# Kernel tuning notes

Measured on AMD Instinct MI355X. Metric: run time of the kernel, lower is better.

Reference implementation:

```python
import jax, jax.numpy as jnp
import numpy as np

EPS = 1e-4  # BatchNorm eps from module


def setup_inputs() -> dict:
    key = jax.random.key(0)
    ks = jax.random.split(key, 7)
    N, C, H, W = 4, 256, 64, 64
    D = C  # reduction=1
    x = jax.random.normal(ks[0], (N, C, H, W), dtype=jnp.float32)
    # 1x1 conv weights, msra-style scaled init
    s = 1.0 / np.sqrt(C)
    Wq = jax.random.normal(ks[1], (D, C), dtype=jnp.float32) * s
    Wk = jax.random.normal(ks[2], (D, C), dtype=jnp.float32) * s
    Wv = jax.random.normal(ks[3], (D, C), dtype=jnp.float32) * s
    Wo = jax.random.normal(ks[4], (C, D), dtype=jnp.float32) * s
    gamma = jnp.ones((C,), dtype=jnp.float32)
    beta = jnp.zeros((C,), dtype=jnp.float32)
    return {"x": x, "Wq": Wq, "Wk": Wk, "Wv": Wv, "Wo": Wo, "gamma": gamma, "beta": beta}


def reference(x, Wq, Wk, Wv, Wo, gamma, beta):
    N, C, H, W = x.shape
    D = Wq.shape[0]
    scale = 1.0 / jnp.sqrt(jnp.float32(D))
    xf = x.reshape(N, C, H * W)                      # (N, C, L)
    # 1x1 convs == per-position linear projections
    q = jnp.einsum('dc,ncl->nld', Wq, xf)            # (N, L, D)
    k = jnp.einsum('dc,ncl->nld', Wk, xf)            # (N, L, D)
    v = jnp.einsum('dc,ncl->nld', Wv, xf)            # (N, L, D)
    scores = jnp.einsum('nld,nmd->nlm', q, k) * scale  # (N, L, L)
    attn = jax.nn.softmax(scores, axis=2)
    out = jnp.einsum('nlm,nmd->nld', attn, v)        # (N, L, D)
    out = jnp.einsum('od,nld->nol', Wo, out).reshape(N, C, H, W)
    # BatchNorm2d (training-mode batch statistics, biased variance)
    mean = jnp.mean(out, axis=(0, 2, 3), keepdims=True)
    var = jnp.var(out, axis=(0, 2, 3), keepdims=True)
    out = (out - mean) * jax.lax.rsqrt(var + EPS)
    out = out * gamma[None, :, None, None] + beta[None, :, None, None]
    return x + out
```

## Files before the change

kernel.cpp:

```cpp
#include <hip/hip_runtime.h>
#include <cstdint>
#include <cstddef>

#define NB 4
#define CH 256
#define LL 4096

typedef unsigned short u16;
typedef unsigned int u32;
typedef unsigned char u8;
typedef __attribute__((ext_vector_type(8))) short bf16x8;
typedef __attribute__((ext_vector_type(4))) float f32x4;
typedef __attribute__((ext_vector_type(16))) float f32x16;

#define GPTR(p) ((const __attribute__((address_space(1))) u32*)(p))
#define LPTR(p) ((__attribute__((address_space(3))) u32*)(p))

__device__ __forceinline__ float blo(u32 x) { return __uint_as_float(x << 16); }
__device__ __forceinline__ float bhi(u32 x) { return __uint_as_float(x & 0xffff0000u); }
__device__ __forceinline__ float b2f(u16 h) { return __uint_as_float(((u32)h) << 16); }
__device__ __forceinline__ u16 f2b(float f) {
    u32 u = __float_as_uint(f);
    u32 r = (u + 0x7fffu + ((u >> 16) & 1u)) >> 16;
    return (u16)r;
}
__device__ __forceinline__ u32 pack2(float a, float b) {
    return (u32)f2b(a) | ((u32)f2b(b) << 16);
}

__global__ __launch_bounds__(256) void prep_kernel(
    const float* __restrict__ x, const float* __restrict__ Wq,
    const float* __restrict__ Wk, const float* __restrict__ Wv,
    const float* __restrict__ Wo, u16* __restrict__ Wb,
    float* __restrict__ stats, u16* __restrict__ xT) {
    const int id = blockIdx.x;
    const int tid = threadIdx.x;
    __shared__ u16 t[64][72];
    if (id < 1024) {
        const int n = id >> 8;
        const int c0 = ((id >> 6) & 3) * 64, l0 = (id & 63) * 64;
        const float* xs = x + (size_t)n * CH * LL;
        const int lq = (tid & 15) * 4, cc = tid >> 4;
#pragma unroll
        for (int p = 0; p < 4; ++p) {
            int c = cc + p * 16;
            float4 v = *(const float4*)&xs[(size_t)(c0 + c) * LL + l0 + lq];
            t[lq + 0][c] = f2b(v.x);
            t[lq + 1][c] = f2b(v.y);
            t[lq + 2][c] = f2b(v.z);
            t[lq + 3][c] = f2b(v.w);
        }
        __syncthreads();
        u16* xo = xT + (size_t)n * LL * CH;
        const int l = tid >> 2, c8 = (tid & 3) * 16;
#pragma unroll
        for (int h = 0; h < 2; ++h) {
            uint4 vv = *(uint4*)&t[l][c8 + h * 8];
            *(uint4*)&xo[(size_t)(l0 + l) * CH + c0 + c8 + h * 8] = vv;
        }
    } else {
        const int j = id - 1024;
        const int i = (j & 63) * 256 + tid;
        const int m = j >> 6;
        if (m == 0 && (j & 63) < 2) stats[i] = 0.0f;
        const float* src = (m == 0) ? Wq : (m == 1) ? Wk : (m == 2) ? Wv : Wo;
        float4 v = ((const float4*)src)[i];
        uint2 o;
        o.x = pack2(v.x, v.y);
        o.y = pack2(v.z, v.w);
        ((uint2*)(Wb + m * 65536))[i] = o;
    }
}

__global__ __launch_bounds__(256, 2) void proj_kernel(
    const u16* __restrict__ xT, const u16* __restrict__ Wb,
    u16* __restrict__ q, u16* __restrict__ k, u16* __restrict__ vT) {
    const int id = blockIdx.x;
    const int tid = threadIdx.x;
    const int w = tid >> 6, lane = tid & 63;
    const int lhi = lane >> 4, llo = lane & 15;

    __shared__ __align__(16) u16 Bs[128 * 256];

    if (id < 1024) {
        const int n = id >> 8;
        const int yy = (id >> 6) & 3;
        const int dhalf = yy & 1, mat = yy >> 1;
        const int l0 = (id & 63) * 64;
        const int d0 = dhalf * 128;

        const u16* xn = xT + (size_t)n * LL * CH;
        const u16* Wm = Wb + mat * 65536 + (size_t)d0 * CH;

#pragma unroll
        for (int i = 0; i < 16; ++i) {
            int s = i * 256 + tid;
            int r = s >> 5, c = s & 31;
            __builtin_amdgcn_global_load_lds(GPTR(Wm + r * CH + (c ^ (r & 31)) * 8),
                                             LPTR((char*)Bs + i * 4096 + w * 1024),
                                             16, 0, 0);
        }

        bf16x8 af[8];
        const u16* abase = xn + (size_t)(l0 + w * 16 + llo) * CH + lhi * 8;
#pragma unroll
        for (int ks = 0; ks < 8; ++ks) af[ks] = *(const bf16x8*)(abase + ks * 32);

        f32x4 acc[8];
#pragma unroll
        for (int t = 0; t < 8; ++t) acc[t] = (f32x4){0.f, 0.f, 0.f, 0.f};

        __syncthreads();

#pragma unroll
        for (int ks = 0; ks < 8; ++ks) {
#pragma unroll
            for (int ct = 0; ct < 8; ++ct) {
                const int rr = ct * 16 + llo;
                bf16x8 bf = *(const bf16x8*)(Bs + rr * CH +
                                             ((ks * 4 + lhi) ^ (rr & 31)) * 8);
                acc[ct] = __builtin_amdgcn_mfma_f32_16x16x32_bf16(af[ks], bf, acc[ct], 0, 0, 0);
            }
        }

        u16* o = (mat ? k : q) + (size_t)n * LL * CH;
#pragma unroll
        for (int r = 0; r < 4; ++r) {
            int lr = l0 + w * 16 + lhi * 4 + r;
#pragma unroll
            for (int ct = 0; ct < 8; ++ct)
                o[(size_t)lr * CH + d0 + ct * 16 + llo] = f2b(acc[ct][r]);
        }
    } else {
        const int j = id - 1024;
        const int n = j >> 7;
        const int d0 = ((j >> 5) & 3) * 64;
        const int l0 = (j & 31) * 128;

        const u16* xn = xT + (size_t)n * LL * CH + (size_t)l0 * CH;
        const u16* Wm = Wb + 2 * 65536;

#pragma unroll
        for (int i = 0; i < 16; ++i) {
            int s = i * 256 + tid;
            int r = s >> 5, c = s & 31;
            __builtin_amdgcn_global_load_lds(GPTR(xn + r * CH + (c ^ (r & 31)) * 8),
                                             LPTR((char*)Bs + i * 4096 + w * 1024),
                                             16, 0, 0);
        }

        bf16x8 af[8];
        const u16* abase = Wm + (size_t)(d0 + w * 16 + llo) * CH + lhi * 8;
#pragma unroll
        for (int ks = 0; ks < 8; ++ks) af[ks] = *(const bf16x8*)(abase + ks * 32);

        f32x4 acc[8];
#pragma unroll
        for (int t = 0; t < 8; ++t) acc[t] = (f32x4){0.f, 0.f, 0.f, 0.f};

        __syncthreads();

#pragma unroll
        for (int ks = 0; ks < 8; ++ks) {
#pragma unroll
            for (int ct = 0; ct < 8; ++ct) {
                const int rr = ct * 16 + llo;
                bf16x8 bf = *(const bf16x8*)(Bs + rr * CH +
                                             ((ks * 4 + lhi) ^ (rr & 31)) * 8);
                acc[ct] = __builtin_amdgcn_mfma_f32_16x16x32_bf16(af[ks], bf, acc[ct], 0, 0, 0);
            }
        }

        u16* o = vT + (size_t)n * CH * LL;
#pragma unroll
        for (int r = 0; r < 4; ++r) {
            int dr = d0 + w * 16 + lhi * 4 + r;
#pragma unroll
            for (int ct = 0; ct < 8; ++ct)
                o[(size_t)dr * LL + l0 + ct * 16 + llo] = f2b(acc[ct][r]);
        }
    }
}

__global__ __launch_bounds__(256, 2) void fattn_kernel(
    const u16* __restrict__ q, const u16* __restrict__ k,
    const u16* __restrict__ vT, u16* __restrict__ Op, float* __restrict__ l_s,
    int iters) {
    const int n = blockIdx.y;
    const int s_id = blockIdx.z;
    const int l0 = blockIdx.x * 128;
    const int m_base = s_id * iters * 32;
    const int tid = threadIdx.x;
    const int w = tid >> 6;
    const int lane = tid & 63;
    const int l31 = lane & 31;
    const int h = lane >> 5;

    __shared__ __align__(16) char smem[65536];

    bf16x8 qf[16];
    {
        const u16* base = q + (size_t)(n * LL + l0 + w * 32 + l31) * CH + h * 8;
#pragma unroll
        for (int s = 0; s < 16; ++s) qf[s] = *(const bf16x8*)(base + s * 16);
    }

    const u16* kg = k + (size_t)n * LL * CH;
    const u16* vg = vT + (size_t)n * CH * LL;

    int okK[4], okV[4];
#pragma unroll
    for (int i = 0; i < 4; ++i) {
        int s = i * 256 + tid;
        int rK = s >> 5;
        int cK = (s & 31) ^ rK;
        okK[i] = rK * CH + cK * 8;
        int dV = s >> 2;
        int cV = (s & 3) ^ ((dV & 3) ^ ((dV >> 2) & 3));
        okV[i] = dV * LL + cV * 8;
    }

    f32x16 oacc[8];
#pragma unroll
    for (int t = 0; t < 8; ++t)
        oacc[t] = (f32x16){0.f, 0.f, 0.f, 0.f, 0.f, 0.f, 0.f, 0.f,
                           0.f, 0.f, 0.f, 0.f, 0.f, 0.f, 0.f, 0.f};
    float lrun = 0.f;

    const float C1 = 0.09016844005556021f;
    const int kx = h ^ l31;
    const int hg = h ^ ((lane & 3) ^ ((lane >> 2) & 3));

    {
        const u16* kg2 = kg + (size_t)m_base * CH;
        const u16* vg2 = vg + m_base;
#pragma unroll
        for (int i = 0; i < 4; ++i) {
            __builtin_amdgcn_global_load_lds(GPTR(kg2 + okK[i]),
                                             LPTR(smem + i * 4096 + w * 1024), 16, 0, 0);
            __builtin_amdgcn_global_load_lds(GPTR(vg2 + okV[i]),
                                             LPTR(smem + 32768 + i * 4096 + w * 1024),
                                             16, 0, 0);
        }
    }

    for (int it = 0; it < iters; ++it) {
        __syncthreads();
        if (it + 1 < iters) {
            const int m1 = m_base + (it + 1) * 32;
            const u16* kg2 = kg + (size_t)m1 * CH;
            const u16* vg2 = vg + m1;
            char* Kb = smem + ((it + 1) & 1) * 16384;
            char* Vb = smem + 32768 + ((it + 1) & 1) * 16384;
#pragma unroll
            for (int i = 0; i < 4; ++i) {
                __builtin_amdgcn_global_load_lds(GPTR(kg2 + okK[i]),
                                                 LPTR(Kb + i * 4096 + w * 1024), 16, 0, 0);
                __builtin_amdgcn_global_load_lds(GPTR(vg2 + okV[i]),
                                                 LPTR(Vb + i * 4096 + w * 1024), 16, 0, 0);
            }
        }
        const u16* Kl = (const u16*)(smem + (it & 1) * 16384);
        const u16* Vl = (const u16*)(smem + 32768 + (it & 1) * 16384);

        f32x16 sacc = (f32x16){0.f, 0.f, 0.f, 0.f, 0.f, 0.f, 0.f, 0.f,
                               0.f, 0.f, 0.f, 0.f, 0.f, 0.f, 0.f, 0.f};
        __builtin_amdgcn_s_setprio(1);
#pragma unroll
        for (int s = 0; s < 16; ++s) {
            bf16x8 af = *(const bf16x8*)(Kl + l31 * 256 + ((2 * s) ^ kx) * 8);
            sacc = __builtin_amdgcn_mfma_f32_32x32x16_bf16(af, qf[s], sacc, 0, 0, 0);
        }
        __builtin_amdgcn_s_setprio(0);

        u32 W[4][2];
#pragma unroll
        for (int g = 0; g < 4; ++g) {
            float p0 = __builtin_amdgcn_exp2f(sacc[4 * g + 0] * C1);
            float p1 = __builtin_amdgcn_exp2f(sacc[4 * g + 1] * C1);
            float p2 = __builtin_amdgcn_exp2f(sacc[4 * g + 2] * C1);
            float p3 = __builtin_amdgcn_exp2f(sacc[4 * g + 3] * C1);
            lrun += (p0 + p1) + (p2 + p3);
            asm("v_cvt_pk_bf16_f32 %0, %1, %2" : "=v"(W[g][0]) : "v"(p0), "v"(p1));
            asm("v_cvt_pk_bf16_f32 %0, %1, %2" : "=v"(W[g][1]) : "v"(p2), "v"(p3));
        }

        bf16x8 pa[2];
#pragma unroll
        for (int sp = 0; sp < 2; ++sp) {
            u32 a0 = W[2 * sp][0], b0 = W[2 * sp + 1][0];
            asm("v_permlane32_swap_b32 %0, %1" : "+v"(a0), "+v"(b0));
            u32 a1 = W[2 * sp][1], b1 = W[2 * sp + 1][1];
            asm("v_permlane32_swap_b32 %0, %1" : "+v"(a1), "+v"(b1));
            union { u32 u[4]; bf16x8 v; } pk;
            pk.u[0] = a0;
            pk.u[1] = a1;
            pk.u[2] = b0;
            pk.u[3] = b1;
            pa[sp] = pk.v;
        }

        __builtin_amdgcn_s_setprio(1);
#pragma unroll
        for (int sp = 0; sp < 2; ++sp) {
#pragma unroll
            for (int dt = 0; dt < 8; ++dt) {
                bf16x8 vf = *(const bf16x8*)(Vl + (dt * 32 + l31) * 32 +
                                             ((2 * sp) ^ hg) * 8);
                oacc[dt] = __builtin_amdgcn_mfma_f32_32x32x16_bf16(pa[sp], vf, oacc[dt], 0, 0, 0);
            }
        }
        __builtin_amdgcn_s_setprio(0);
    }

    u16* ap = Op + (size_t)((s_id * NB + n) * (size_t)LL + l0 + w * 32) * CH;
    float* lp = l_s + (size_t)s_id * NB * LL + (size_t)n * LL + l0 + w * 32;
    lrun += __shfl_xor(lrun, 32);
    if (h == 0) lp[l31] = lrun;
#pragma unroll
    for (int dt = 0; dt < 8; ++dt) {
#pragma unroll
        for (int r = 0; r < 16; ++r) {
            int qrow = (r & 3) + 8 * (r >> 2) + 4 * h;
            ap[(size_t)qrow * CH + dt * 32 + l31] = f2b(oacc[dt][r]);
        }
    }
}

__global__ __launch_bounds__(256) void merge_kernel(
    const u16* __restrict__ Op, const float* __restrict__ l_s,
    u16* __restrict__ att, int S) {
    const size_t t8 = (size_t)blockIdx.x * 256 + threadIdx.x;
    const size_t flat = t8 * 8;
    const size_t row = flat >> 8;
    float lsum = 0.0f;
    for (int s = 0; s < S; ++s) lsum += l_s[(size_t)s * NB * LL + row];
    const float inv = 1.0f / lsum;
    float acc[8];
#pragma unroll
    for (int j = 0; j < 8; ++j) acc[j] = 0.0f;
    for (int s = 0; s < S; ++s) {
        uint4 raw = *(const uint4*)(Op + (size_t)s * NB * LL * CH + flat);
        acc[0] += blo(raw.x); acc[1] += bhi(raw.x);
        acc[2] += blo(raw.y); acc[3] += bhi(raw.y);
        acc[4] += blo(raw.z); acc[5] += bhi(raw.z);
        acc[6] += blo(raw.w); acc[7] += bhi(raw.w);
    }
    uint4 o;
    o.x = pack2(acc[0] * inv, acc[1] * inv);
    o.y = pack2(acc[2] * inv, acc[3] * inv);
    o.z = pack2(acc[4] * inv, acc[5] * inv);
    o.w = pack2(acc[6] * inv, acc[7] * inv);
    *(uint4*)(att + flat) = o;
}

__global__ __launch_bounds__(256, 2) void outm_kernel(
    const u16* __restrict__ Wb, const u16* __restrict__ att,
    u16* __restrict__ y, float* __restrict__ stats) {
    const int n = blockIdx.z;
    const int o0 = blockIdx.y * 64;
    const int l0 = blockIdx.x * 128;
    const int tid = threadIdx.x;
    const int w = tid >> 6, lane = tid & 63;
    const int lhi = lane >> 4, llo = lane & 15;

    __shared__ __align__(16) u16 Bs[128 * 256];

    const u16* an = att + (size_t)n * LL * CH + (size_t)l0 * CH;
    const u16* Wm = Wb + 3 * 65536;

#pragma unroll
    for (int i = 0; i < 16; ++i) {
        int s = i * 256 + tid;
        int r = s >> 5, c = s & 31;
        __builtin_amdgcn_global_load_lds(GPTR(an + r * CH + (c ^ (r & 31)) * 8),
                                         LPTR((char*)Bs + i * 4096 + w * 1024),
                                         16, 0, 0);
    }

    bf16x8 af[8];
    const u16* abase = Wm + (size_t)(o0 + w * 16 + llo) * CH + lhi * 8;
#pragma unroll
    for (int ks = 0; ks < 8; ++ks) af[ks] = *(const bf16x8*)(abase + ks * 32);

    f32x4 acc[8];
#pragma unroll
    for (int t = 0; t < 8; ++t) acc[t] = (f32x4){0.f, 0.f, 0.f, 0.f};

    __syncthreads();

#pragma unroll
    for (int ks = 0; ks < 8; ++ks) {
#pragma unroll
        for (int ct = 0; ct < 8; ++ct) {
            const int rr = ct * 16 + llo;
            bf16x8 bf = *(const bf16x8*)(Bs + rr * CH +
                                         ((ks * 4 + lhi) ^ (rr & 31)) * 8);
            acc[ct] = __builtin_amdgcn_mfma_f32_16x16x32_bf16(af[ks], bf, acc[ct], 0, 0, 0);
        }
    }

    u16* yn = y + (size_t)n * CH * LL;
#pragma unroll
    for (int r = 0; r < 4; ++r) {
        const int orow = o0 + w * 16 + lhi * 4 + r;
        float ts = 0.0f, tq = 0.0f;
#pragma unroll
        for (int ct = 0; ct < 8; ++ct) {
            float vv = acc[ct][r];
            yn[(size_t)orow * LL + l0 + ct * 16 + llo] = f2b(vv);
            ts += vv;
            tq += vv * vv;
        }
        ts += __shfl_xor(ts, 1); tq += __shfl_xor(tq, 1);
        ts += __shfl_xor(ts, 2); tq += __shfl_xor(tq, 2);
        ts += __shfl_xor(ts, 4); tq += __shfl_xor(tq, 4);
        ts += __shfl_xor(ts, 8); tq += __shfl_xor(tq, 8);
        if (llo == 0) {
            atomicAdd(&stats[orow], ts);
            atomicAdd(&stats[256 + orow], tq);
        }
    }
}

__global__ __launch_bounds__(256) void bn_kernel(
    const float* __restrict__ x, const u16* __restrict__ y,
    const float* __restrict__ stats, const float* __restrict__ gamma,
    const float* __restrict__ beta, float* __restrict__ out) {
    const int idx = blockIdx.x * 256 + threadIdx.x;
    const int base = idx * 4;
    const int c = (base >> 12) & 255;
    const float cnt = 1.0f / 16384.0f;
    float mean = stats[c] * cnt;
    float var = stats[256 + c] * cnt - mean * mean;
    float rstd = rsqrtf(var + 1e-4f);
    float g = gamma[c] * rstd;
    float b = beta[c];
    uint2 yv = ((const uint2*)y)[idx];
    float4 xv = ((const float4*)x)[idx];
    float4 o;
    o.x = xv.x + (blo(yv.x) - mean) * g + b;
    o.y = xv.y + (bhi(yv.x) - mean) * g + b;
    o.z = xv.z + (blo(yv.y) - mean) * g + b;
    o.w = xv.w + (bhi(yv.y) - mean) * g + b;
    ((float4*)out)[idx] = o;
}

extern "C" void kernel_launch(void* const* d_in, const int* in_sizes, int n_in,
                              void* d_out, int out_size, void* d_ws, size_t ws_size,
                              hipStream_t stream) {
    const float* x = (const float*)d_in[0];
    const float* Wq = (const float*)d_in[1];
    const float* Wk = (const float*)d_in[2];
    const float* Wv = (const float*)d_in[3];
    const float* Wo = (const float*)d_in[4];
    const float* gamma = (const float*)d_in[5];
    const float* beta = (const float*)d_in[6];
    float* out = (float*)d_out;

    const size_t elems = (size_t)NB * LL * CH;

    int S = 1;
    for (int cand = 4; cand >= 2; cand >>= 1) {
        size_t need = elems * 2 * (size_t)(3 + cand) +
                      (size_t)cand * NB * LL * 4 + 524288 + 8192;
        if (ws_size >= need) { S = cand; break; }
    }
    const int iters = 128 / S;

    char* wsb = (char*)d_ws;
    u16* q = (u16*)wsb;
    u16* k = q + elems;
    u16* vT = k + elems;
    u16* Op = vT + elems;
    u16* xT = Op;
    float* l_s = (float*)(Op + (size_t)S * elems);
    u16* Wb = (u16*)(l_s + (size_t)S * NB * LL);
    float* stats = (float*)(Wb + 4 * 65536);
    u16* att = q;
    u16* y = k;

    prep_kernel<<<1280, 256, 0, stream>>>(x, Wq, Wk, Wv, Wo, Wb, stats, xT);
    proj_kernel<<<1536, 256, 0, stream>>>(xT, Wb, q, k, vT);
    fattn_kernel<<<dim3(LL / 128, NB, S), 256, 0, stream>>>(q, k, vT, Op, l_s, iters);
    merge_kernel<<<(int)(elems / 8 / 256), 256, 0, stream>>>(Op, l_s, att, S);
    outm_kernel<<<dim3(LL / 128, CH / 64, NB), 256, 0, stream>>>(Wb, att, y, stats);
    bn_kernel<<<(NB * CH * LL / 4) / 256, 256, 0, stream>>>(x, y, stats, gamma, beta, out);
}
```

Baseline: 197.4 us.

## Fuse split-K attention merge into output projection kernel

Removes the separate merge kernel and performs the split partial-sum reduction and normalization inside the output projection kernel, writing the merged tile straight into shared memory. The output projection now processes 32 positions per block across all 256 output channels, looping over four 64-channel groups, so the merged attention tensor no longer round-trips through global memory and one launch is saved. In exchange each block reloads the full Wo weights and issues four times as many stats atomics per element row, with smaller MFMA tiles per block.

```diff
diff --git a/kernel.cpp b/kernel.cpp
--- a/kernel.cpp
+++ b/kernel.cpp
@@ -327,98 +327,92 @@
     }
 }
 
-__global__ __launch_bounds__(256) void merge_kernel(
-    const u16* __restrict__ Op, const float* __restrict__ l_s,
-    u16* __restrict__ att, int S) {
-    const size_t t8 = (size_t)blockIdx.x * 256 + threadIdx.x;
-    const size_t flat = t8 * 8;
-    const size_t row = flat >> 8;
-    float lsum = 0.0f;
-    for (int s = 0; s < S; ++s) lsum += l_s[(size_t)s * NB * LL + row];
-    const float inv = 1.0f / lsum;
-    float acc[8];
-#pragma unroll
-    for (int j = 0; j < 8; ++j) acc[j] = 0.0f;
-    for (int s = 0; s < S; ++s) {
-        uint4 raw = *(const uint4*)(Op + (size_t)s * NB * LL * CH + flat);
-        acc[0] += blo(raw.x); acc[1] += bhi(raw.x);
-        acc[2] += blo(raw.y); acc[3] += bhi(raw.y);
-        acc[4] += blo(raw.z); acc[5] += bhi(raw.z);
-        acc[6] += blo(raw.w); acc[7] += bhi(raw.w);
-    }
-    uint4 o;
-    o.x = pack2(acc[0] * inv, acc[1] * inv);
-    o.y = pack2(acc[2] * inv, acc[3] * inv);
-    o.z = pack2(acc[4] * inv, acc[5] * inv);
-    o.w = pack2(acc[6] * inv, acc[7] * inv);
-    *(uint4*)(att + flat) = o;
-}
-
 __global__ __launch_bounds__(256, 2) void outm_kernel(
-    const u16* __restrict__ Wb, const u16* __restrict__ att,
-    u16* __restrict__ y, float* __restrict__ stats) {
-    const int n = blockIdx.z;
-    const int o0 = blockIdx.y * 64;
-    const int l0 = blockIdx.x * 128;
+    const u16* __restrict__ Wb, const u16* __restrict__ Op,
+    const float* __restrict__ l_s, u16* __restrict__ y,
+    float* __restrict__ stats, int S) {
+    const int n = blockIdx.y;
+    const int l0 = blockIdx.x * 32;
     const int tid = threadIdx.x;
     const int w = tid >> 6, lane = tid & 63;
     const int lhi = lane >> 4, llo = lane & 15;
 
-    __shared__ __align__(16) u16 Bs[128 * 256];
-
-    const u16* an = att + (size_t)n * LL * CH + (size_t)l0 * CH;
+    __shared__ __align__(16) u16 Bs[32 * 256];
+
     const u16* Wm = Wb + 3 * 65536;
-
-#pragma unroll
-    for (int i = 0; i < 16; ++i) {
+    const size_t opbase = (size_t)n * LL * CH + (size_t)l0 * CH;
+    const size_t sstride = (size_t)NB * LL * CH;
+
+#pragma unroll
+    for (int i = 0; i < 4; ++i) {
         int s = i * 256 + tid;
         int r = s >> 5, c = s & 31;
-        __builtin_amdgcn_global_load_lds(GPTR(an + r * CH + (c ^ (r & 31)) * 8),
-                                         LPTR((char*)Bs + i * 4096 + w * 1024),
-                                         16, 0, 0);
-    }
-
-    bf16x8 af[8];
-    const u16* abase = Wm + (size_t)(o0 + w * 16 + llo) * CH + lhi * 8;
-#pragma unroll
-    for (int ks = 0; ks < 8; ++ks) af[ks] = *(const bf16x8*)(abase + ks * 32);
-
-    f32x4 acc[8];
-#pragma unroll
-    for (int t = 0; t < 8; ++t) acc[t] = (f32x4){0.f, 0.f, 0.f, 0.f};
+        const u16* src = Op + opbase + (size_t)r * CH + (c ^ r) * 8;
+        float lsum = 0.0f;
+        for (int sp = 0; sp < S; ++sp)
+            lsum += l_s[(size_t)sp * NB * LL + (size_t)n * LL + l0 + r];
+        const float inv = 1.0f / lsum;
+        float acc[8];
+#pragma unroll
+        for (int j = 0; j < 8; ++j) acc[j] = 0.0f;
+        for (int sp = 0; sp < S; ++sp) {
+            uint4 raw = *(const uint4*)(src + (size_t)sp * sstride);
+            acc[0] += blo(raw.x); acc[1] += bhi(raw.x);
+            acc[2] += blo(raw.y); acc[3] += bhi(raw.y);
+            acc[4] += blo(raw.z); acc[5] += bhi(raw.z);
+            acc[6] += blo(raw.w); acc[7] += bhi(raw.w);
+        }
+        uint4 o;
+        o.x = pack2(acc[0] * inv, acc[1] * inv);
+        o.y = pack2(acc[2] * inv, acc[3] * inv);
+        o.z = pack2(acc[4] * inv, acc[5] * inv);
+        o.w = pack2(acc[6] * inv, acc[7] * inv);
+        *(uint4*)(Bs + (size_t)s * 8) = o;
+    }
 
     __syncthreads();
 
-#pragma unroll
-    for (int ks = 0; ks < 8; ++ks) {
-#pragma unroll
-        for (int ct = 0; ct < 8; ++ct) {
-            const int rr = ct * 16 + llo;
-            bf16x8 bf = *(const bf16x8*)(Bs + rr * CH +
-                                         ((ks * 4 + lhi) ^ (rr & 31)) * 8);
-            acc[ct] = __builtin_amdgcn_mfma_f32_16x16x32_bf16(af[ks], bf, acc[ct], 0, 0, 0);
-        }
-    }
-
     u16* yn = y + (size_t)n * CH * LL;
 #pragma unroll
-    for (int r = 0; r < 4; ++r) {
-        const int orow = o0 + w * 16 + lhi * 4 + r;
-        float ts = 0.0f, tq = 0.0f;
-#pragma unroll
-        for (int ct = 0; ct < 8; ++ct) {
-            float vv = acc[ct][r];
-            yn[(size_t)orow * LL + l0 + ct * 16 + llo] = f2b(vv);
-            ts += vv;
-            tq += vv * vv;
-        }
-        ts += __shfl_xor(ts, 1); tq += __shfl_xor(tq, 1);
-        ts += __shfl_xor(ts, 2); tq += __shfl_xor(tq, 2);
-        ts += __shfl_xor(ts, 4); tq += __shfl_xor(tq, 4);
-        ts += __shfl_xor(ts, 8); tq += __shfl_xor(tq, 8);
-        if (llo == 0) {
-            atomicAdd(&stats[orow], ts);
-            atomicAdd(&stats[256 + orow], tq);
+    for (int o0 = 0; o0 < 4; ++o0) {
+        bf16x8 af[8];
+        const u16* abase = Wm + (size_t)(o0 * 64 + w * 16 + llo) * CH + lhi * 8;
+#pragma unroll
+        for (int ks = 0; ks < 8; ++ks) af[ks] = *(const bf16x8*)(abase + ks * 32);
+
+        f32x4 acc[2];
+        acc[0] = (f32x4){0.f, 0.f, 0.f, 0.f};
+        acc[1] = (f32x4){0.f, 0.f, 0.f, 0.f};
+#pragma unroll
+        for (int ks = 0; ks < 8; ++ks) {
+#pragma unroll
+            for (int ct = 0; ct < 2; ++ct) {
+                const int rr = ct * 16 + llo;
+                bf16x8 bf = *(const bf16x8*)(Bs + rr * CH +
+                                             ((ks * 4 + lhi) ^ rr) * 8);
+                acc[ct] = __builtin_amdgcn_mfma_f32_16x16x32_bf16(af[ks], bf, acc[ct], 0, 0, 0);
+            }
+        }
+
+#pragma unroll
+        for (int r = 0; r < 4; ++r) {
+            const int orow = o0 * 64 + w * 16 + lhi * 4 + r;
+            float ts = 0.0f, tq = 0.0f;
+#pragma unroll
+            for (int ct = 0; ct < 2; ++ct) {
+                float vv = acc[ct][r];
+                yn[(size_t)orow * LL + l0 + ct * 16 + llo] = f2b(vv);
+                ts += vv;
+                tq += vv * vv;
+            }
+            ts += __shfl_xor(ts, 1); tq += __shfl_xor(tq, 1);
+            ts += __shfl_xor(ts, 2); tq += __shfl_xor(tq, 2);
+            ts += __shfl_xor(ts, 4); tq += __shfl_xor(tq, 4);
+            ts += __shfl_xor(ts, 8); tq += __shfl_xor(tq, 8);
+            if (llo == 0) {
+                atomicAdd(&stats[orow], ts);
+                atomicAdd(&stats[256 + orow], tq);
+            }
         }
     }
 }
@@ -477,13 +471,11 @@
     float* l_s = (float*)(Op + (size_t)S * elems);
     u16* Wb = (u16*)(l_s + (size_t)S * NB * LL);
     float* stats = (float*)(Wb + 4 * 65536);
-    u16* att = q;
     u16* y = k;
 
     prep_kernel<<<1280, 256, 0, stream>>>(x, Wq, Wk, Wv, Wo, Wb, stats, xT);
     proj_kernel<<<1536, 256, 0, stream>>>(xT, Wb, q, k, vT);
     fattn_kernel<<<dim3(LL / 128, NB, S), 256, 0, stream>>>(q, k, vT, Op, l_s, iters);
-    merge_kernel<<<(int)(elems / 8 / 256), 256, 0, stream>>>(Op, l_s, att, S);
-    outm_kernel<<<dim3(LL / 128, CH / 64, NB), 256, 0, stream>>>(Wb, att, y, stats);
+    outm_kernel<<<dim3(LL / 32, NB), 256, 0, stream>>>(Wb, Op, l_s, y, stats, S);
     bn_kernel<<<(NB * CH * LL / 4) / 256, 256, 0, stream>>>(x, y, stats, gamma, beta, out);
 }
```

Result: slower. 273.6 us (+38.6%).
